# Kernel optimization log

Hardware: AMD Instinct MI355X
Metric: run time of the kernel (lower is better)

The kernel has to match this reference:

```python
import jax, jax.numpy as jnp
import numpy as np

B, S, H = 2, 2048, 2048
E, I, TOPK = 8, 1408, 2


def setup_inputs() -> dict:
    key = jax.random.key(0)
    k0, k1, k2, k3, k4 = jax.random.split(key, 5)
    return {
        "hidden_states": jax.random.normal(k0, (B, S, H), dtype=jnp.float32),
        "Wr": jax.random.normal(k1, (H, E), dtype=jnp.float32) * 0.02,
        "Wg": jax.random.normal(k2, (E, H, I), dtype=jnp.float32) * 0.02,
        "Wu": jax.random.normal(k3, (E, H, I), dtype=jnp.float32) * 0.02,
        "Wd": jax.random.normal(k4, (E, I, H), dtype=jnp.float32) * 0.02,
    }


def reference(hidden_states, Wr, Wg, Wu, Wd):
    b, s, h = hidden_states.shape
    x = hidden_states.reshape(-1, h)                      # [T, H]
    T = x.shape[0]
    router_logits = x @ Wr                                # [T, E]
    probs = jax.nn.softmax(router_logits.astype(jnp.float32), axis=-1)
    top_w, top_i = jax.lax.top_k(probs, TOPK)             # [T, k]
    top_w = top_w / jnp.sum(top_w, axis=-1, keepdims=True)  # norm_topk_prob
    top_w = top_w.astype(x.dtype)
    # combine weights per (token, expert): zero where expert not selected
    cw = jnp.zeros((T, E), dtype=x.dtype).at[
        jnp.arange(T)[:, None], top_i].add(top_w)         # [T, E]
    # per-expert SwiGLU MLP computed densely, masked/weighted by cw
    g = jax.nn.silu(jnp.einsum('th,ehi->tei', x, Wg))     # [T, E, I]
    u = jnp.einsum('th,ehi->tei', x, Wu)                  # [T, E, I]
    y = jnp.einsum('tei,eih->teh', g * u, Wd)             # [T, E, H]
    out = jnp.einsum('te,teh->th', cw, y)                 # [T, H]
    return out.reshape(b, s, h), router_logits
```

## Files before the change

kernel.cpp:

```cpp
#include <hip/hip_runtime.h>

#define T_TOK 4096
#define HD 2048
#define NE 8
#define NI 1408

typedef __bf16 bf16x8 __attribute__((ext_vector_type(8)));
typedef float f32x4 __attribute__((ext_vector_type(4)));

#define S_WAITCNT_VMCNT(n) asm volatile("s_waitcnt vmcnt(" #n ")" ::: "memory")
__device__ __forceinline__ void wave_barrier() {
  asm volatile("" ::: "memory");
  __builtin_amdgcn_s_barrier();
  asm volatile("" ::: "memory");
}

__device__ __forceinline__ unsigned short f2bf(float f) {
  unsigned int u = __float_as_uint(f);
  u += 0x7FFFu + ((u >> 16) & 1u);
  return (unsigned short)(u >> 16);
}

__device__ __forceinline__ void gload_lds16(const void* g, void* l) {
  __builtin_amdgcn_global_load_lds(
      (const __attribute__((address_space(1))) unsigned int*)g,
      (__attribute__((address_space(3))) unsigned int*)l, 16, 0, 0);
}

__global__ void transpose_cvt_kernel(const float* __restrict__ src,
                                     unsigned short* __restrict__ dst,
                                     int R, int C) {
  __shared__ float tile[64][33];
  int e = blockIdx.z;
  int c0 = blockIdx.x * 32, r0 = blockIdx.y * 64;
  int tid = threadIdx.x;
  int tx = tid & 31, rr = tid >> 5;
  const float* s = src + (size_t)e * R * C;
  unsigned short* d = dst + (size_t)e * R * C;
#pragma unroll
  for (int j = 0; j < 8; j++) {
    int r = rr + j * 8;
    tile[r][tx] = s[(size_t)(r0 + r) * C + c0 + tx];
  }
  __syncthreads();
  int l32 = tid & 31, cb = tid >> 5;
#pragma unroll
  for (int j = 0; j < 4; j++) {
    int c = cb + j * 8;
    ushort2 v = { f2bf(tile[2 * l32][c]), f2bf(tile[2 * l32 + 1][c]) };
    ((ushort2*)(d + (size_t)(c0 + c) * R + r0))[l32] = v;
  }
}

__global__ void router_kernel(const float* __restrict__ x,
                              const float* __restrict__ Wr,
                              float* __restrict__ logits,
                              unsigned short* __restrict__ xbf,
                              int4* __restrict__ tokinfo,
                              int* __restrict__ cnt) {
  int wv = threadIdx.x >> 6, lane = threadIdx.x & 63;
  int t = blockIdx.x * 4 + wv;
  const float* xr = x + (size_t)t * HD;
  unsigned short* xbr = xbf + (size_t)t * HD;
  float acc[NE];
#pragma unroll
  for (int e = 0; e < NE; e++) acc[e] = 0.f;
  for (int hi = 0; hi < HD / 64; hi++) {
    int h = hi * 64 + lane;
    float xv = xr[h];
    xbr[h] = f2bf(xv);
    const float4* w4 = (const float4*)(Wr + (size_t)h * NE);
    float4 a = w4[0], b = w4[1];
    acc[0] += xv * a.x; acc[1] += xv * a.y; acc[2] += xv * a.z; acc[3] += xv * a.w;
    acc[4] += xv * b.x; acc[5] += xv * b.y; acc[6] += xv * b.z; acc[7] += xv * b.w;
  }
#pragma unroll
  for (int m = 32; m > 0; m >>= 1) {
#pragma unroll
    for (int e = 0; e < NE; e++) acc[e] += __shfl_xor(acc[e], m, 64);
  }
  if (lane < NE) logits[(size_t)t * NE + lane] = acc[lane];
  if (lane == 0) {
    int e0 = 0;
#pragma unroll
    for (int e = 1; e < NE; e++) if (acc[e] > acc[e0]) e0 = e;
    int e1 = (e0 == 0) ? 1 : 0;
#pragma unroll
    for (int e = 0; e < NE; e++) if (e != e0 && acc[e] > acc[e1]) e1 = e;
    float ex = expf(acc[e1] - acc[e0]);
    float w0 = 1.f / (1.f + ex);
    float w1 = ex / (1.f + ex);
    atomicAdd(&cnt[e0], 1);
    atomicAdd(&cnt[e1], 1);
    tokinfo[t] = make_int4(e0, e1, __float_as_int(w0), __float_as_int(w1));
  }
}

__global__ void offsets_kernel(int* __restrict__ cnt) {
  int o = 0;
  for (int e = 0; e < NE; e++) { cnt[8 + e] = o; o += cnt[e]; }
}

__global__ void scatter_kernel(const int4* __restrict__ tokinfo,
                               int* __restrict__ cnt,
                               int* __restrict__ row_tok,
                               float* __restrict__ row_w) {
  int t = blockIdx.x * blockDim.x + threadIdx.x;
  if (t >= T_TOK) return;
  int4 info = tokinfo[t];
  int p0 = atomicAdd(&cnt[16 + info.x], 1);
  int r0 = cnt[8 + info.x] + p0;
  row_tok[r0] = t; row_w[r0] = __int_as_float(info.z);
  int p1 = atomicAdd(&cnt[16 + info.y], 1);
  int r1 = cnt[8 + info.y] + p1;
  row_tok[r1] = t; row_w[r1] = __int_as_float(info.w);
}

__launch_bounds__(256, 2)
__global__ void gemm1_kernel(const unsigned short* __restrict__ xbf,
                             const unsigned short* __restrict__ Wgt,
                             const unsigned short* __restrict__ Wut,
                             unsigned short* __restrict__ act,
                             const int* __restrict__ row_tok,
                             const int* __restrict__ cnt) {
  const int f = blockIdx.x + 11 * (blockIdx.y + 32 * blockIdx.z);
  const int e = f & 7;
  const int rem = f >> 3;
  const int nt = rem >> 5;
  const int mt = rem & 31;
  const int c = cnt[e];
  if (mt * 128 >= c) return;
  const int off = cnt[8 + e];
  const int rowbase = off + mt * 128, rowend = off + c;
  const int i0 = nt * 128;
  __shared__ __align__(16) char smem[49152];
  const int lane = threadIdx.x & 63, w = threadIdx.x >> 6;
  const int wr = w >> 1, wc = w & 1;

  const int rr0 = w * 16 + (lane >> 2);
  const int rr1 = rr0 + 64;
  const int q0 = (lane & 3) ^ ((rr0 >> 1) & 3);
  const int q1 = (lane & 3) ^ ((rr1 >> 1) & 3);
  int g0 = rowbase + rr0; if (g0 > rowend - 1) g0 = rowend - 1;
  int g1 = rowbase + rr1; if (g1 > rowend - 1) g1 = rowend - 1;
  const size_t tokA0 = (size_t)row_tok[g0] * HD;
  const size_t tokA1 = (size_t)row_tok[g1] * HD;
  const size_t bB0 = ((size_t)e * NI + i0 + rr0) * HD;
  const size_t bB1 = ((size_t)e * NI + i0 + rr1) * HD;
  const int ldsA = w * 1024;

  f32x4 zero = {0.f, 0.f, 0.f, 0.f};
  f32x4 accg[4][4], accu[4][4];
#pragma unroll
  for (int a = 0; a < 4; a++)
#pragma unroll
    for (int b = 0; b < 4; b++) { accg[a][b] = zero; accu[a][b] = zero; }

  auto stage = [&](int buf, int ks) {
    const int k0 = ks * 32;
    char* base = smem + buf * 24576;
    gload_lds16(xbf + tokA0 + k0 + q0 * 8, base + ldsA);
    gload_lds16(xbf + tokA1 + k0 + q1 * 8, base + ldsA + 4096);
    gload_lds16(Wgt + bB0 + k0 + q0 * 8, base + 8192 + ldsA);
    gload_lds16(Wgt + bB1 + k0 + q1 * 8, base + 8192 + ldsA + 4096);
    gload_lds16(Wut + bB0 + k0 + q0 * 8, base + 16384 + ldsA);
    gload_lds16(Wut + bB1 + k0 + q1 * 8, base + 16384 + ldsA + 4096);
  };
  const int rl = lane & 15, kslot = lane >> 4;
  auto compute = [&](int buf) {
    const char* base = smem + buf * 24576;
    bf16x8 af[4], bg[4], bu[4];
#pragma unroll
    for (int mi = 0; mi < 4; mi++) {
      int r = wr * 64 + mi * 16 + rl;
      int byt = r * 64 + ((kslot ^ ((r >> 1) & 3)) << 4);
      af[mi] = *(const bf16x8*)(base + byt);
    }
#pragma unroll
    for (int ni = 0; ni < 4; ni++) {
      int r = wc * 64 + ni * 16 + rl;
      int byt = r * 64 + ((kslot ^ ((r >> 1) & 3)) << 4);
      bg[ni] = *(const bf16x8*)(base + 8192 + byt);
      bu[ni] = *(const bf16x8*)(base + 16384 + byt);
    }
#pragma unroll
    for (int mi = 0; mi < 4; mi++)
#pragma unroll
      for (int ni = 0; ni < 4; ni++) {
        accg[mi][ni] = __builtin_amdgcn_mfma_f32_16x16x32_bf16(af[mi], bg[ni], accg[mi][ni], 0, 0, 0);
        accu[mi][ni] = __builtin_amdgcn_mfma_f32_16x16x32_bf16(af[mi], bu[ni], accu[mi][ni], 0, 0, 0);
      }
  };

  stage(0, 0);
  const int NKS = HD / 32;
  int ks = 0;
  for (; ks < NKS - 1; ks++) {
    stage((ks + 1) & 1, ks + 1);
    S_WAITCNT_VMCNT(6);
    wave_barrier();
    compute(ks & 1);
    wave_barrier();
  }
  S_WAITCNT_VMCNT(0);
  wave_barrier();
  compute(ks & 1);

  const int rh = lane >> 4;
#pragma unroll
  for (int mi = 0; mi < 4; mi++)
#pragma unroll
    for (int ni = 0; ni < 4; ni++)
#pragma unroll
      for (int j = 0; j < 4; j++) {
        int grow = rowbase + wr * 64 + mi * 16 + rh * 4 + j;
        if (grow < rowend) {
          int gcol = i0 + wc * 64 + ni * 16 + rl;
          float g = accg[mi][ni][j], u = accu[mi][ni][j];
          float val = g / (1.f + __expf(-g)) * u;
          act[(size_t)grow * NI + gcol] = f2bf(val);
        }
      }
}

__launch_bounds__(256, 2)
__global__ void gemm2_kernel(const unsigned short* __restrict__ act,
                             const unsigned short* __restrict__ Wdt,
                             float* __restrict__ out,
                             const int* __restrict__ row_tok,
                             const float* __restrict__ row_w,
                             const int* __restrict__ cnt) {
  const int f = blockIdx.x + 16 * (blockIdx.y + 32 * blockIdx.z);
  const int e = f & 7;
  const int rem = f >> 3;
  const int nt = rem >> 5;
  const int mt = rem & 31;
  const int c = cnt[e];
  if (mt * 128 >= c) return;
  const int off = cnt[8 + e];
  const int rowbase = off + mt * 128, rowend = off + c;
  const int n0 = nt * 128;
  __shared__ __align__(16) char smem[32768];
  const int lane = threadIdx.x & 63, w = threadIdx.x >> 6;
  const int wr = w >> 1, wc = w & 1;

  const int rr0 = w * 16 + (lane >> 2);
  const int rr1 = rr0 + 64;
  const int q0 = (lane & 3) ^ ((rr0 >> 1) & 3);
  const int q1 = (lane & 3) ^ ((rr1 >> 1) & 3);
  int g0 = rowbase + rr0; if (g0 > rowend - 1) g0 = rowend - 1;
  int g1 = rowbase + rr1; if (g1 > rowend - 1) g1 = rowend - 1;
  const size_t aA0 = (size_t)g0 * NI;
  const size_t aA1 = (size_t)g1 * NI;
  const size_t bB0 = ((size_t)e * HD + n0 + rr0) * NI;
  const size_t bB1 = ((size_t)e * HD + n0 + rr1) * NI;
  const int ldsA = w * 1024;

  f32x4 zero = {0.f, 0.f, 0.f, 0.f};
  f32x4 acc[4][4];
#pragma unroll
  for (int a = 0; a < 4; a++)
#pragma unroll
    for (int b = 0; b < 4; b++) acc[a][b] = zero;

  auto stage = [&](int buf, int ks) {
    const int k0 = ks * 32;
    char* base = smem + buf * 16384;
    gload_lds16(act + aA0 + k0 + q0 * 8, base + ldsA);
    gload_lds16(act + aA1 + k0 + q1 * 8, base + ldsA + 4096);
    gload_lds16(Wdt + bB0 + k0 + q0 * 8, base + 8192 + ldsA);
    gload_lds16(Wdt + bB1 + k0 + q1 * 8, base + 8192 + ldsA + 4096);
  };
  const int rl = lane & 15, kslot = lane >> 4;
  auto compute = [&](int buf) {
    const char* base = smem + buf * 16384;
    bf16x8 af[4], bf[4];
#pragma unroll
    for (int mi = 0; mi < 4; mi++) {
      int r = wr * 64 + mi * 16 + rl;
      int byt = r * 64 + ((kslot ^ ((r >> 1) & 3)) << 4);
      af[mi] = *(const bf16x8*)(base + byt);
    }
#pragma unroll
    for (int ni = 0; ni < 4; ni++) {
      int r = wc * 64 + ni * 16 + rl;
      int byt = r * 64 + ((kslot ^ ((r >> 1) & 3)) << 4);
      bf[ni] = *(const bf16x8*)(base + 8192 + byt);
    }
#pragma unroll
    for (int mi = 0; mi < 4; mi++)
#pragma unroll
      for (int ni = 0; ni < 4; ni++)
        acc[mi][ni] = __builtin_amdgcn_mfma_f32_16x16x32_bf16(af[mi], bf[ni], acc[mi][ni], 0, 0, 0);
  };

  stage(0, 0);
  const int NKS = NI / 32;
  int ks = 0;
  for (; ks < NKS - 1; ks++) {
    stage((ks + 1) & 1, ks + 1);
    S_WAITCNT_VMCNT(4);
    wave_barrier();
    compute(ks & 1);
    wave_barrier();
  }
  S_WAITCNT_VMCNT(0);
  wave_barrier();
  compute(ks & 1);

  const int rh = lane >> 4;
#pragma unroll
  for (int mi = 0; mi < 4; mi++)
#pragma unroll
    for (int ni = 0; ni < 4; ni++)
#pragma unroll
      for (int j = 0; j < 4; j++) {
        int grow = rowbase + wr * 64 + mi * 16 + rh * 4 + j;
        if (grow < rowend) {
          int t = row_tok[grow];
          float wgt = row_w[grow];
          int gcol = n0 + wc * 64 + ni * 16 + rl;
          unsafeAtomicAdd(&out[(size_t)t * HD + gcol], wgt * acc[mi][ni][j]);
        }
      }
}

extern "C" void kernel_launch(void* const* d_in, const int* in_sizes, int n_in,
                              void* d_out, int out_size, void* d_ws, size_t ws_size,
                              hipStream_t stream) {
  const float* x  = (const float*)d_in[0];
  const float* Wr = (const float*)d_in[1];
  const float* Wg = (const float*)d_in[2];
  const float* Wu = (const float*)d_in[3];
  const float* Wd = (const float*)d_in[4];
  float* out = (float*)d_out;
  char* ws = (char*)d_ws;

  unsigned short* xbf = (unsigned short*)(ws);
  unsigned short* Wgt = (unsigned short*)(ws + 16777216);
  unsigned short* Wut = (unsigned short*)(ws + 62914560);
  unsigned short* Wdt = (unsigned short*)(ws + 109051904);
  unsigned short* act = (unsigned short*)(ws + 155189248);
  int4*  tokinfo      = (int4*)(ws + 178257920);
  int*   row_tok      = (int*)(ws + 178323456);
  float* row_w        = (float*)(ws + 178356224);
  int*   cnt          = (int*)(ws + 178388992);

  hipMemsetAsync(out, 0, (size_t)T_TOK * HD * sizeof(float), stream);
  hipMemsetAsync(cnt, 0, 96, stream);

  router_kernel<<<T_TOK / 4, 256, 0, stream>>>(x, Wr, out + (size_t)T_TOK * HD, xbf, tokinfo, cnt);
  offsets_kernel<<<1, 1, 0, stream>>>(cnt);
  scatter_kernel<<<T_TOK / 256, 256, 0, stream>>>(tokinfo, cnt, row_tok, row_w);

  transpose_cvt_kernel<<<dim3(NI / 32, HD / 64, NE), 256, 0, stream>>>(Wg, Wgt, HD, NI);
  transpose_cvt_kernel<<<dim3(NI / 32, HD / 64, NE), 256, 0, stream>>>(Wu, Wut, HD, NI);
  transpose_cvt_kernel<<<dim3(HD / 32, NI / 64, NE), 256, 0, stream>>>(Wd, Wdt, NI, HD);

  gemm1_kernel<<<dim3(11, 32, NE), 256, 0, stream>>>(xbf, Wgt, Wut, act, row_tok, cnt);
  gemm2_kernel<<<dim3(16, 32, NE), 256, 0, stream>>>(act, Wdt, out, row_tok, row_w, cnt);
}
```

Before: 528.7 us.

## Replace atomic scatter-add with bf16 expert output buffer and combine kernel

gemm2 now writes each expert row's result as bf16 into a dense buffer, which reuses the Wgt region since Wgt is no longer needed after gemm1. A new combine kernel gathers each token's two rows and applies the routing weights. This removes the memset of the output and the fp32 atomic adds into it. The weight transpose-convert kernel also moves to 64x64 tiles with float4 loads and 16-byte bf16 stores, and gemm2's launch bounds ask for 3 blocks per SIMD. The cost is an extra kernel launch, an extra round trip through the intermediate buffer, and bf16 rounding of the expert outputs.

```diff
diff --git a/kernel.cpp b/kernel.cpp
--- a/kernel.cpp
+++ b/kernel.cpp
@@ -7,6 +7,7 @@
 
 typedef __bf16 bf16x8 __attribute__((ext_vector_type(8)));
 typedef float f32x4 __attribute__((ext_vector_type(4)));
+typedef unsigned short ushort8 __attribute__((ext_vector_type(8)));
 
 #define S_WAITCNT_VMCNT(n) asm volatile("s_waitcnt vmcnt(" #n ")" ::: "memory")
 __device__ __forceinline__ void wave_barrier() {
@@ -20,6 +21,9 @@
   u += 0x7FFFu + ((u >> 16) & 1u);
   return (unsigned short)(u >> 16);
 }
+__device__ __forceinline__ float bf2f(unsigned short u) {
+  return __uint_as_float((unsigned int)u << 16);
+}
 
 __device__ __forceinline__ void gload_lds16(const void* g, void* l) {
   __builtin_amdgcn_global_load_lds(
@@ -30,25 +34,29 @@
 __global__ void transpose_cvt_kernel(const float* __restrict__ src,
                                      unsigned short* __restrict__ dst,
                                      int R, int C) {
-  __shared__ float tile[64][33];
+  __shared__ float tile[64][65];
   int e = blockIdx.z;
-  int c0 = blockIdx.x * 32, r0 = blockIdx.y * 64;
-  int tid = threadIdx.x;
-  int tx = tid & 31, rr = tid >> 5;
+  int r0 = blockIdx.y * 64, c0 = blockIdx.x * 64;
   const float* s = src + (size_t)e * R * C;
   unsigned short* d = dst + (size_t)e * R * C;
-#pragma unroll
-  for (int j = 0; j < 8; j++) {
-    int r = rr + j * 8;
-    tile[r][tx] = s[(size_t)(r0 + r) * C + c0 + tx];
+  int tid = threadIdx.x;
+  int lr = tid >> 4, lc = (tid & 15) * 4;
+#pragma unroll
+  for (int p = 0; p < 4; p++) {
+    int r = lr + p * 16;
+    float4 v = *(const float4*)(s + (size_t)(r0 + r) * C + c0 + lc);
+    tile[r][lc] = v.x; tile[r][lc + 1] = v.y;
+    tile[r][lc + 2] = v.z; tile[r][lc + 3] = v.w;
   }
   __syncthreads();
-  int l32 = tid & 31, cb = tid >> 5;
-#pragma unroll
-  for (int j = 0; j < 4; j++) {
-    int c = cb + j * 8;
-    ushort2 v = { f2bf(tile[2 * l32][c]), f2bf(tile[2 * l32 + 1][c]) };
-    ((ushort2*)(d + (size_t)(c0 + c) * R + r0))[l32] = v;
+  int rbase = (tid & 7) * 8, crel = tid >> 3;
+#pragma unroll
+  for (int p = 0; p < 2; p++) {
+    int c = p * 32 + crel;
+    ushort8 o;
+#pragma unroll
+    for (int j = 0; j < 8; j++) o[j] = f2bf(tile[rbase + j][c]);
+    *(ushort8*)(d + (size_t)(c0 + c) * R + r0 + rbase) = o;
   }
 }
 
@@ -104,16 +112,17 @@
 __global__ void scatter_kernel(const int4* __restrict__ tokinfo,
                                int* __restrict__ cnt,
                                int* __restrict__ row_tok,
-                               float* __restrict__ row_w) {
+                               int2* __restrict__ tok2row) {
   int t = blockIdx.x * blockDim.x + threadIdx.x;
   if (t >= T_TOK) return;
   int4 info = tokinfo[t];
   int p0 = atomicAdd(&cnt[16 + info.x], 1);
   int r0 = cnt[8 + info.x] + p0;
-  row_tok[r0] = t; row_w[r0] = __int_as_float(info.z);
+  row_tok[r0] = t;
   int p1 = atomicAdd(&cnt[16 + info.y], 1);
   int r1 = cnt[8 + info.y] + p1;
-  row_tok[r1] = t; row_w[r1] = __int_as_float(info.w);
+  row_tok[r1] = t;
+  tok2row[t] = make_int2(r0, r1);
 }
 
 __launch_bounds__(256, 2)
@@ -223,12 +232,10 @@
       }
 }
 
-__launch_bounds__(256, 2)
+__launch_bounds__(256, 3)
 __global__ void gemm2_kernel(const unsigned short* __restrict__ act,
                              const unsigned short* __restrict__ Wdt,
-                             float* __restrict__ out,
-                             const int* __restrict__ row_tok,
-                             const float* __restrict__ row_w,
+                             unsigned short* __restrict__ y,
                              const int* __restrict__ cnt) {
   const int f = blockIdx.x + 16 * (blockIdx.y + 32 * blockIdx.z);
   const int e = f & 7;
@@ -317,12 +324,33 @@
       for (int j = 0; j < 4; j++) {
         int grow = rowbase + wr * 64 + mi * 16 + rh * 4 + j;
         if (grow < rowend) {
-          int t = row_tok[grow];
-          float wgt = row_w[grow];
           int gcol = n0 + wc * 64 + ni * 16 + rl;
-          unsafeAtomicAdd(&out[(size_t)t * HD + gcol], wgt * acc[mi][ni][j]);
+          y[(size_t)grow * HD + gcol] = f2bf(acc[mi][ni][j]);
         }
       }
+}
+
+__global__ void combine_kernel(const unsigned short* __restrict__ y,
+                               const int2* __restrict__ tok2row,
+                               const int4* __restrict__ tokinfo,
+                               float* __restrict__ out) {
+  int t = blockIdx.x, tid = threadIdx.x;
+  int2 rr = tok2row[t];
+  int4 info = tokinfo[t];
+  float w0 = __int_as_float(info.z), w1 = __int_as_float(info.w);
+  ushort8 a = ((const ushort8*)(y + (size_t)rr.x * HD))[tid];
+  ushort8 b = ((const ushort8*)(y + (size_t)rr.y * HD))[tid];
+  float4 o0, o1;
+  o0.x = w0 * bf2f(a[0]) + w1 * bf2f(b[0]);
+  o0.y = w0 * bf2f(a[1]) + w1 * bf2f(b[1]);
+  o0.z = w0 * bf2f(a[2]) + w1 * bf2f(b[2]);
+  o0.w = w0 * bf2f(a[3]) + w1 * bf2f(b[3]);
+  o1.x = w0 * bf2f(a[4]) + w1 * bf2f(b[4]);
+  o1.y = w0 * bf2f(a[5]) + w1 * bf2f(b[5]);
+  o1.z = w0 * bf2f(a[6]) + w1 * bf2f(b[6]);
+  o1.w = w0 * bf2f(a[7]) + w1 * bf2f(b[7]);
+  float4* op = (float4*)(out + (size_t)t * HD + tid * 8);
+  op[0] = o0; op[1] = o1;
 }
 
 extern "C" void kernel_launch(void* const* d_in, const int* in_sizes, int n_in,
@@ -341,22 +369,23 @@
   unsigned short* Wut = (unsigned short*)(ws + 62914560);
   unsigned short* Wdt = (unsigned short*)(ws + 109051904);
   unsigned short* act = (unsigned short*)(ws + 155189248);
+  unsigned short* yb  = (unsigned short*)(ws + 16777216);
   int4*  tokinfo      = (int4*)(ws + 178257920);
   int*   row_tok      = (int*)(ws + 178323456);
-  float* row_w        = (float*)(ws + 178356224);
+  int2*  tok2row      = (int2*)(ws + 178356224);
   int*   cnt          = (int*)(ws + 178388992);
 
-  hipMemsetAsync(out, 0, (size_t)T_TOK * HD * sizeof(float), stream);
   hipMemsetAsync(cnt, 0, 96, stream);
 
   router_kernel<<<T_TOK / 4, 256, 0, stream>>>(x, Wr, out + (size_t)T_TOK * HD, xbf, tokinfo, cnt);
   offsets_kernel<<<1, 1, 0, stream>>>(cnt);
-  scatter_kernel<<<T_TOK / 256, 256, 0, stream>>>(tokinfo, cnt, row_tok, row_w);
-
-  transpose_cvt_kernel<<<dim3(NI / 32, HD / 64, NE), 256, 0, stream>>>(Wg, Wgt, HD, NI);
-  transpose_cvt_kernel<<<dim3(NI / 32, HD / 64, NE), 256, 0, stream>>>(Wu, Wut, HD, NI);
-  transpose_cvt_kernel<<<dim3(HD / 32, NI / 64, NE), 256, 0, stream>>>(Wd, Wdt, NI, HD);
+  scatter_kernel<<<T_TOK / 256, 256, 0, stream>>>(tokinfo, cnt, row_tok, tok2row);
+
+  transpose_cvt_kernel<<<dim3(NI / 64, HD / 64, NE), 256, 0, stream>>>(Wg, Wgt, HD, NI);
+  transpose_cvt_kernel<<<dim3(NI / 64, HD / 64, NE), 256, 0, stream>>>(Wu, Wut, HD, NI);
+  transpose_cvt_kernel<<<dim3(HD / 64, NI / 64, NE), 256, 0, stream>>>(Wd, Wdt, NI, HD);
 
   gemm1_kernel<<<dim3(11, 32, NE), 256, 0, stream>>>(xbf, Wgt, Wut, act, row_tok, cnt);
-  gemm2_kernel<<<dim3(16, 32, NE), 256, 0, stream>>>(act, Wdt, out, row_tok, row_w, cnt);
-}
+  gemm2_kernel<<<dim3(16, 32, NE), 256, 0, stream>>>(act, Wdt, yb, cnt);
+  combine_kernel<<<T_TOK, 256, 0, stream>>>(yb, tok2row, tokinfo, out);
+}
```

Measured after the change: 459.9 us. 13.0% less time.
